# Kernel tuning notes

Measured on AMD Instinct MI355X. Metric: run time of the kernel, lower is better.

Reference implementation:

```python
import jax, jax.numpy as jnp
import numpy as np

LN_EPS = 1e-5
BN_EPS = 1e-5


def setup_inputs() -> dict:
    key = jax.random.key(0)
    ks = jax.random.split(key, 16)
    N, C, T, H, W = 4, 256, 5, 28, 28
    Ci = 128
    CA = 128  # audio feature dim (hard-coded 128 in nn.Linear(128, in_channels))
    s = 0.02
    inp = {
        "x": jax.random.normal(ks[0], (N, C, T, H, W), jnp.float32),
        "audio": jax.random.normal(ks[1], (N, T, CA), jnp.float32),
        "align_W": jax.random.normal(ks[2], (C, CA), jnp.float32) * s,
        "align_b": jax.random.normal(ks[3], (C,), jnp.float32) * s,
        "g_W": jax.random.normal(ks[4], (Ci, C), jnp.float32) * s,
        "g_b": jax.random.normal(ks[5], (Ci,), jnp.float32) * s,
        "theta_W": jax.random.normal(ks[6], (Ci, C), jnp.float32) * s,
        "theta_b": jax.random.normal(ks[7], (Ci,), jnp.float32) * s,
        "phi_W": jax.random.normal(ks[8], (Ci, C), jnp.float32) * s,
        "phi_b": jax.random.normal(ks[9], (Ci,), jnp.float32) * s,
        "Wz_W": jax.random.normal(ks[10], (C, Ci), jnp.float32) * s,
        "Wz_b": jax.random.normal(ks[11], (C,), jnp.float32) * s,
        "bn_gamma": jax.random.normal(ks[12], (C,), jnp.float32) * s + 1.0,
        "bn_beta": jax.random.normal(ks[13], (C,), jnp.float32) * s,
        "bn_mean": jnp.zeros((C,), jnp.float32),
        "bn_var": jnp.ones((C,), jnp.float32),
        "ln_gamma": jnp.ones((C,), jnp.float32),
        "ln_beta": jnp.zeros((C,), jnp.float32),
    }
    return inp


def _tpavi(x, audio, align_W, align_b, g_W, g_b, theta_W, theta_b,
           phi_W, phi_b, Wz_W, Wz_b, bn_gamma, bn_beta, bn_mean, bn_var,
           ln_gamma, ln_beta):
    N, C, T, H, W = x.shape
    L = T * H * W
    # audio alignment: Linear(128 -> C), then broadcast over H, W
    audio_temp = jnp.einsum('ntc,oc->nto', audio, align_W) + align_b     # (N,T,C)
    a = audio_temp.transpose(0, 2, 1)[:, :, :, None, None]               # (N,C,T,1,1)
    a = jnp.broadcast_to(a, (N, C, T, H, W)).reshape(N, C, L)            # (N,C,L)

    xf = x.reshape(N, C, L)                                              # (N,C,L)
    # 1x1 conv3d == per-token channel mixing
    g_x = jnp.einsum('oc,ncl->nlo', g_W, xf) + g_b                       # (N,L,Ci)
    theta_x = jnp.einsum('oc,ncl->nlo', theta_W, xf) + theta_b           # (N,L,Ci)
    phi_x = jnp.einsum('oc,ncl->nol', phi_W, a) + phi_b[None, :, None]   # (N,Ci,L)

    # dot mode: f = theta phi^T, normalized by token count (no softmax)
    f = jnp.einsum('nlo,nok->nlk', theta_x, phi_x)                       # (N,L,L)
    f_div_C = f / L
    y = jnp.einsum('nlk,nko->nlo', f_div_C, g_x)                         # (N,L,Ci)

    y = y.transpose(0, 2, 1)                                             # (N,Ci,L)
    # W_z: 1x1 conv (Ci -> C) + BatchNorm3d (inference statistics)
    wy = jnp.einsum('oc,ncl->nol', Wz_W, y) + Wz_b[None, :, None]        # (N,C,L)
    inv = bn_gamma / jnp.sqrt(bn_var + BN_EPS)
    wy = (wy - bn_mean[None, :, None]) * inv[None, :, None] + bn_beta[None, :, None]

    z = wy.reshape(N, C, T, H, W) + x                                    # residual
    # LayerNorm over channel dim (channels-last in the original)
    zt = z.transpose(0, 2, 3, 4, 1)                                      # (N,T,H,W,C)
    mu = jnp.mean(zt, axis=-1, keepdims=True)
    var = jnp.mean(jnp.square(zt - mu), axis=-1, keepdims=True)
    zt = (zt - mu) / jnp.sqrt(var + LN_EPS) * ln_gamma + ln_beta
    z = zt.transpose(0, 4, 1, 2, 3)                                      # (N,C,T,H,W)
    return z, audio_temp


def reference(x, audio, align_W, align_b, g_W, g_b, theta_W, theta_b,
              phi_W, phi_b, Wz_W, Wz_b, bn_gamma, bn_beta, bn_mean, bn_var,
              ln_gamma, ln_beta):
    return _tpavi(x, audio, align_W, align_b, g_W, g_b, theta_W, theta_b,
                  phi_W, phi_b, Wz_W, Wz_b, bn_gamma, bn_beta, bn_mean, bn_var,
                  ln_gamma, ln_beta)
```

## Files before the change

### kernel.cpp

```cpp
#include <hip/hip_runtime.h>

#define N_DIM 4
#define C_DIM 256
#define T_DIM 5
#define HW    784
#define L_TOK 3920
#define CI    128
#define CA    128

#define WS_XS   0
#define WS_TR   8192

__global__ __launch_bounds__(256) void kA(const float* __restrict__ x,
                                          const float* __restrict__ align_W,
                                          const float* __restrict__ phi_W,
                                          const float* __restrict__ g_W,
                                          const float* __restrict__ Wz_W,
                                          float* __restrict__ ws) {
    int bid = blockIdx.x;
    int tid = threadIdx.x;
    if (bid < N_DIM * C_DIM * T_DIM) {
        int n   = bid / (C_DIM * T_DIM);
        int rem = bid % (C_DIM * T_DIM);
        int c   = rem / T_DIM;
        int t   = rem % T_DIM;
        const float4* base = (const float4*)(x + ((size_t)(n * C_DIM + c) * T_DIM + t) * HW);
        float p = 0.f;
        if (tid < HW / 4) {
            float4 v = base[tid];
            p = (v.x + v.y) + (v.z + v.w);
        }
        for (int off = 32; off > 0; off >>= 1) p += __shfl_down(p, off, 64);
        __shared__ float wsum[4];
        if ((tid & 63) == 0) wsum[tid >> 6] = p;
        __syncthreads();
        if (tid == 0)
            ws[WS_XS + (n * T_DIM + t) * C_DIM + c] = wsum[0] + wsum[1] + wsum[2] + wsum[3];
    } else {
        int tb = bid - N_DIM * C_DIM * T_DIM;
        #pragma unroll
        for (int k = 0; k < 4; ++k) {
            int D = tb * 1024 + k * 256 + tid;
            int m = D >> 15;
            int r = D & 32767;
            float v;
            if (m == 0)      { int a = r >> 8, c = r & 255; v = align_W[c * CA + a]; }
            else if (m == 1) { int c = r >> 7, o = r & 127; v = phi_W[o * C_DIM + c]; }
            else if (m == 2) { int c = r >> 7, o = r & 127; v = g_W[o * C_DIM + c]; }
            else             { int o = r >> 8, c = r & 255; v = Wz_W[c * CI + o]; }
            ws[WS_TR + D] = v;
        }
    }
}

__global__ __launch_bounds__(1024) void kB(
    const float* __restrict__ x,        const float* __restrict__ ws,
    const float* __restrict__ audio,    const float* __restrict__ align_b,
    const float* __restrict__ g_b,      const float* __restrict__ theta_W,
    const float* __restrict__ theta_b,  const float* __restrict__ phi_b,
    const float* __restrict__ Wz_b,     const float* __restrict__ bn_gamma,
    const float* __restrict__ bn_beta,  const float* __restrict__ bn_mean,
    const float* __restrict__ bn_var,   const float* __restrict__ ln_gamma,
    const float* __restrict__ ln_beta,  float* __restrict__ out,
    float* __restrict__ out_audio) {
    __shared__ float audio_s[T_DIM * CA];
    __shared__ float xs_s[T_DIM * C_DIM];
    __shared__ float at_s[T_DIM * C_DIM];
    __shared__ float phi_s[T_DIM * CI];
    __shared__ float g2_s[T_DIM * CI];
    __shared__ float TPs[T_DIM * C_DIM];
    __shared__ float GWs[T_DIM * C_DIM];
    __shared__ float tb_s[T_DIM];
    __shared__ float B_s[C_DIM], inv_s[C_DIM], lng_s[C_DIM], lnb_s[C_DIM];
    __shared__ float Fp[T_DIM * 1024];
    __shared__ float Sp[2 * 1024];

    int n    = blockIdx.y;
    int tile = blockIdx.x;
    int tid  = threadIdx.x;
    int g    = tid >> 6;
    int li   = tid & 63;
    int l    = tile * 64 + li;
    bool act = (l < L_TOK);

    const float* alignT = ws + WS_TR;
    const float* phiT   = ws + WS_TR + 32768;
    const float* gT     = ws + WS_TR + 65536;
    const float* WzT    = ws + WS_TR + 98304;

    if (tid < T_DIM * CA) audio_s[tid] = audio[n * T_DIM * CA + tid];
    for (int i = tid; i < T_DIM * C_DIM; i += 1024) xs_s[i] = ws[WS_XS + n * T_DIM * C_DIM + i];
    if (tid < C_DIM) {
        int c = tid;
        float inv = bn_gamma[c] * rsqrtf(bn_var[c] + 1e-5f);
        inv_s[c] = inv * (1.0f / (float)L_TOK);
        B_s[c]   = (Wz_b[c] - bn_mean[c]) * inv + bn_beta[c];
        lng_s[c] = ln_gamma[c];
        lnb_s[c] = ln_beta[c];
    }
    __syncthreads();

    for (int i = tid; i < T_DIM * C_DIM; i += 1024) {
        int t = i >> 8, c = i & 255;
        float a0 = 0, a1 = 0, a2 = 0, a3 = 0;
        const float* as = audio_s + t * CA;
        #pragma unroll 8
        for (int a = 0; a < CA; a += 4) {
            a0 = fmaf(alignT[(a + 0) * C_DIM + c], as[a + 0], a0);
            a1 = fmaf(alignT[(a + 1) * C_DIM + c], as[a + 1], a1);
            a2 = fmaf(alignT[(a + 2) * C_DIM + c], as[a + 2], a2);
            a3 = fmaf(alignT[(a + 3) * C_DIM + c], as[a + 3], a3);
        }
        float v = align_b[c] + (a0 + a1) + (a2 + a3);
        at_s[i] = v;
        if (tile == 0) out_audio[n * T_DIM * C_DIM + i] = v;
    }
    __syncthreads();

    if (tid < T_DIM * CI) {
        int t = tid >> 7, o = tid & 127;
        const float* ats = at_s + t * C_DIM;
        const float* xss = xs_s + t * C_DIM;
        float p0 = 0, p1 = 0, q0 = 0, q1 = 0;
        #pragma unroll 8
        for (int c = 0; c < C_DIM; c += 2) {
            p0 = fmaf(phiT[(c + 0) * CI + o], ats[c + 0], p0);
            p1 = fmaf(phiT[(c + 1) * CI + o], ats[c + 1], p1);
            q0 = fmaf(gT[(c + 0) * CI + o],  xss[c + 0], q0);
            q1 = fmaf(gT[(c + 1) * CI + o],  xss[c + 1], q1);
        }
        phi_s[tid] = phi_b[o] + p0 + p1;
        g2_s[tid]  = (float)HW * g_b[o] + q0 + q1;
    }
    __syncthreads();

    for (int i = tid; i < T_DIM * C_DIM; i += 1024) {
        int t = i >> 8, c = i & 255;
        const float* ps = phi_s + t * CI;
        const float* gs = g2_s + t * CI;
        float a0 = 0, a1 = 0, b0 = 0, b1 = 0;
        #pragma unroll 8
        for (int o = 0; o < CI; o += 2) {
            a0 = fmaf(theta_W[(o + 0) * C_DIM + c], ps[o + 0], a0);
            a1 = fmaf(theta_W[(o + 1) * C_DIM + c], ps[o + 1], a1);
            b0 = fmaf(WzT[(o + 0) * C_DIM + c],     gs[o + 0], b0);
            b1 = fmaf(WzT[(o + 1) * C_DIM + c],     gs[o + 1], b1);
        }
        TPs[i] = a0 + a1;
        GWs[i] = (b0 + b1) * inv_s[c];
    }
    if (tid < T_DIM * 64) {
        int t = tid >> 6, lane = tid & 63;
        float p = theta_b[lane] * phi_s[t * CI + lane] +
                  theta_b[lane + 64] * phi_s[t * CI + lane + 64];
        for (int off = 32; off > 0; off >>= 1) p += __shfl_down(p, off, 64);
        if (lane == 0) tb_s[t] = p;
    }
    __syncthreads();

    float xz[16];
    const float* xb = x + ((size_t)(n * C_DIM + g * 16)) * L_TOK + l;
    #pragma unroll
    for (int j = 0; j < 16; ++j) xz[j] = act ? xb[(size_t)j * L_TOK] : 0.f;

    float F0 = 0, F1 = 0, F2 = 0, F3 = 0, F4 = 0;
    #pragma unroll
    for (int j = 0; j < 16; ++j) {
        const float* tp = TPs + g * 16 + j;
        F0 = fmaf(xz[j], tp[0],    F0);
        F1 = fmaf(xz[j], tp[256],  F1);
        F2 = fmaf(xz[j], tp[512],  F2);
        F3 = fmaf(xz[j], tp[768],  F3);
        F4 = fmaf(xz[j], tp[1024], F4);
    }
    Fp[0 * 1024 + tid] = F0; Fp[1 * 1024 + tid] = F1; Fp[2 * 1024 + tid] = F2;
    Fp[3 * 1024 + tid] = F3; Fp[4 * 1024 + tid] = F4;
    __syncthreads();

    float Ft[T_DIM];
    #pragma unroll
    for (int t = 0; t < T_DIM; ++t) {
        float a = tb_s[t];
        #pragma unroll
        for (int w = 0; w < 16; ++w) a += Fp[t * 1024 + w * 64 + li];
        Ft[t] = a;
    }
    float s1 = 0.f, s2 = 0.f;
    #pragma unroll
    for (int j = 0; j < 16; ++j) {
        int c = g * 16 + j;
        float zc = B_s[c] + xz[j];
        zc = fmaf(Ft[0], GWs[c],        zc);
        zc = fmaf(Ft[1], GWs[256 + c],  zc);
        zc = fmaf(Ft[2], GWs[512 + c],  zc);
        zc = fmaf(Ft[3], GWs[768 + c],  zc);
        zc = fmaf(Ft[4], GWs[1024 + c], zc);
        xz[j] = zc;
        s1 += zc;
        s2 = fmaf(zc, zc, s2);
    }
    Sp[tid]        = s1;
    Sp[1024 + tid] = s2;
    __syncthreads();

    float t1 = 0.f, t2 = 0.f;
    #pragma unroll
    for (int w = 0; w < 16; ++w) {
        t1 += Sp[w * 64 + li];
        t2 += Sp[1024 + w * 64 + li];
    }
    float mu   = t1 * (1.0f / C_DIM);
    float var  = t2 * (1.0f / C_DIM) - mu * mu;
    float rstd = rsqrtf(var + 1e-5f);
    if (act) {
        float* ob = out + ((size_t)(n * C_DIM + g * 16)) * L_TOK + l;
        #pragma unroll
        for (int j = 0; j < 16; ++j) {
            int c = g * 16 + j;
            ob[(size_t)j * L_TOK] = fmaf((xz[j] - mu) * rstd, lng_s[c], lnb_s[c]);
        }
    }
}

extern "C" void kernel_launch(void* const* d_in, const int* in_sizes, int n_in,
                              void* d_out, int out_size, void* d_ws, size_t ws_size,
                              hipStream_t stream) {
    const float* x        = (const float*)d_in[0];
    const float* audio    = (const float*)d_in[1];
    const float* align_W  = (const float*)d_in[2];
    const float* align_b  = (const float*)d_in[3];
    const float* g_W      = (const float*)d_in[4];
    const float* g_b      = (const float*)d_in[5];
    const float* theta_W  = (const float*)d_in[6];
    const float* theta_b  = (const float*)d_in[7];
    const float* phi_W    = (const float*)d_in[8];
    const float* phi_b    = (const float*)d_in[9];
    const float* Wz_W     = (const float*)d_in[10];
    const float* Wz_b     = (const float*)d_in[11];
    const float* bn_gamma = (const float*)d_in[12];
    const float* bn_beta  = (const float*)d_in[13];
    const float* bn_mean  = (const float*)d_in[14];
    const float* bn_var   = (const float*)d_in[15];
    const float* ln_gamma = (const float*)d_in[16];
    const float* ln_beta  = (const float*)d_in[17];

    float* out       = (float*)d_out;
    float* out_audio = out + (size_t)N_DIM * C_DIM * L_TOK;
    float* ws        = (float*)d_ws;

    kA<<<N_DIM * C_DIM * T_DIM + 128, 256, 0, stream>>>(x, align_W, phi_W, g_W, Wz_W, ws);
    dim3 gridB((L_TOK + 63) / 64, N_DIM);
    kB<<<gridB, 1024, 0, stream>>>(
        x, ws, audio, align_b, g_b, theta_W, theta_b, phi_b,
        Wz_b, bn_gamma, bn_beta, bn_mean, bn_var, ln_gamma, ln_beta,
        out, out_audio);
}
```

Before: 137.5 us.

## Fuse pre-pass into single cooperative kernel with grid-wide sync

Merges the per-(n,t,c) spatial-sum kernel and weight-transpose kernel into the main kernel, launched cooperatively with 248 blocks. Each block loads its x tile into registers once, reduces per-channel partial sums into workspace split at time-step boundaries, then a grid sync lets every block gather the per-time-step sums. This removes one full extra read of x and a kernel launch. The cost is a grid-wide barrier, a serial 62-tile gather in every block, and a dependency on all blocks being co-resident.

```diff
diff --git a/kernel.cpp b/kernel.cpp
--- a/kernel.cpp
+++ b/kernel.cpp
@@ -1,4 +1,7 @@
 #include <hip/hip_runtime.h>
+#include <hip/hip_cooperative_groups.h>
+
+namespace cg = cooperative_groups;
 
 #define N_DIM 4
 #define C_DIM 256
@@ -7,62 +10,19 @@
 #define L_TOK 3920
 #define CI    128
 #define CA    128
-
-#define WS_XS   0
-#define WS_TR   8192
-
-__global__ __launch_bounds__(256) void kA(const float* __restrict__ x,
-                                          const float* __restrict__ align_W,
-                                          const float* __restrict__ phi_W,
-                                          const float* __restrict__ g_W,
-                                          const float* __restrict__ Wz_W,
-                                          float* __restrict__ ws) {
-    int bid = blockIdx.x;
-    int tid = threadIdx.x;
-    if (bid < N_DIM * C_DIM * T_DIM) {
-        int n   = bid / (C_DIM * T_DIM);
-        int rem = bid % (C_DIM * T_DIM);
-        int c   = rem / T_DIM;
-        int t   = rem % T_DIM;
-        const float4* base = (const float4*)(x + ((size_t)(n * C_DIM + c) * T_DIM + t) * HW);
-        float p = 0.f;
-        if (tid < HW / 4) {
-            float4 v = base[tid];
-            p = (v.x + v.y) + (v.z + v.w);
-        }
-        for (int off = 32; off > 0; off >>= 1) p += __shfl_down(p, off, 64);
-        __shared__ float wsum[4];
-        if ((tid & 63) == 0) wsum[tid >> 6] = p;
-        __syncthreads();
-        if (tid == 0)
-            ws[WS_XS + (n * T_DIM + t) * C_DIM + c] = wsum[0] + wsum[1] + wsum[2] + wsum[3];
-    } else {
-        int tb = bid - N_DIM * C_DIM * T_DIM;
-        #pragma unroll
-        for (int k = 0; k < 4; ++k) {
-            int D = tb * 1024 + k * 256 + tid;
-            int m = D >> 15;
-            int r = D & 32767;
-            float v;
-            if (m == 0)      { int a = r >> 8, c = r & 255; v = align_W[c * CA + a]; }
-            else if (m == 1) { int c = r >> 7, o = r & 127; v = phi_W[o * C_DIM + c]; }
-            else if (m == 2) { int c = r >> 7, o = r & 127; v = g_W[o * C_DIM + c]; }
-            else             { int o = r >> 8, c = r & 255; v = Wz_W[c * CI + o]; }
-            ws[WS_TR + D] = v;
-        }
-    }
-}
-
-__global__ __launch_bounds__(1024) void kB(
-    const float* __restrict__ x,        const float* __restrict__ ws,
-    const float* __restrict__ audio,    const float* __restrict__ align_b,
-    const float* __restrict__ g_b,      const float* __restrict__ theta_W,
-    const float* __restrict__ theta_b,  const float* __restrict__ phi_b,
-    const float* __restrict__ Wz_b,     const float* __restrict__ bn_gamma,
-    const float* __restrict__ bn_beta,  const float* __restrict__ bn_mean,
-    const float* __restrict__ bn_var,   const float* __restrict__ ln_gamma,
-    const float* __restrict__ ln_beta,  float* __restrict__ out,
-    float* __restrict__ out_audio) {
+#define NTILE 62
+
+#define WS_TR   0
+#define WS_XP   131072
+
+struct Args {
+    const float *x, *audio, *align_W, *align_b, *g_W, *g_b, *theta_W, *theta_b,
+                *phi_W, *phi_b, *Wz_W, *Wz_b, *bn_gamma, *bn_beta, *bn_mean,
+                *bn_var, *ln_gamma, *ln_beta;
+    float *ws, *out, *out_audio;
+};
+
+__global__ __launch_bounds__(1024) void kFused(Args A) {
     __shared__ float audio_s[T_DIM * CA];
     __shared__ float xs_s[T_DIM * C_DIM];
     __shared__ float at_s[T_DIM * C_DIM];
@@ -75,30 +35,90 @@
     __shared__ float Fp[T_DIM * 1024];
     __shared__ float Sp[2 * 1024];
 
+    int tile = blockIdx.x;
     int n    = blockIdx.y;
-    int tile = blockIdx.x;
+    int bid  = n * NTILE + tile;
     int tid  = threadIdx.x;
     int g    = tid >> 6;
     int li   = tid & 63;
     int l    = tile * 64 + li;
     bool act = (l < L_TOK);
 
+    float* ws = A.ws;
     const float* alignT = ws + WS_TR;
     const float* phiT   = ws + WS_TR + 32768;
     const float* gT     = ws + WS_TR + 65536;
     const float* WzT    = ws + WS_TR + 98304;
 
-    if (tid < T_DIM * CA) audio_s[tid] = audio[n * T_DIM * CA + tid];
-    for (int i = tid; i < T_DIM * C_DIM; i += 1024) xs_s[i] = ws[WS_XS + n * T_DIM * C_DIM + i];
+    {
+        int gid = bid * 1024 + tid;
+        if (gid < 131072) {
+            int m = gid >> 15;
+            int r = gid & 32767;
+            float v;
+            if (m == 0)      { int a = r >> 8, c = r & 255; v = A.align_W[c * CA + a]; }
+            else if (m == 1) { int c = r >> 7, o = r & 127; v = A.phi_W[o * C_DIM + c]; }
+            else if (m == 2) { int c = r >> 7, o = r & 127; v = A.g_W[o * C_DIM + c]; }
+            else             { int o = r >> 8, c = r & 255; v = A.Wz_W[c * CI + o]; }
+            ws[WS_TR + gid] = v;
+        }
+    }
+
+    if (tid < T_DIM * CA) audio_s[tid] = A.audio[n * T_DIM * CA + tid];
     if (tid < C_DIM) {
         int c = tid;
-        float inv = bn_gamma[c] * rsqrtf(bn_var[c] + 1e-5f);
+        float inv = A.bn_gamma[c] * rsqrtf(A.bn_var[c] + 1e-5f);
         inv_s[c] = inv * (1.0f / (float)L_TOK);
-        B_s[c]   = (Wz_b[c] - bn_mean[c]) * inv + bn_beta[c];
-        lng_s[c] = ln_gamma[c];
-        lnb_s[c] = ln_beta[c];
-    }
-    __syncthreads();
+        B_s[c]   = (A.Wz_b[c] - A.bn_mean[c]) * inv + A.bn_beta[c];
+        lng_s[c] = A.ln_gamma[c];
+        lnb_s[c] = A.ln_beta[c];
+    }
+
+    float xz[16];
+    const float* xb = A.x + ((size_t)(n * C_DIM + g * 16)) * L_TOK + l;
+    #pragma unroll
+    for (int j = 0; j < 16; ++j) xz[j] = act ? xb[(size_t)j * L_TOK] : 0.f;
+
+    {
+        int base = tile * 64;
+        int tlo  = base / HW;
+        int thi  = ((base + 63 < L_TOK) ? (base + 63) : (L_TOK - 1)) / HW;
+        int myl  = act ? l : (L_TOK - 1);
+        int mytt = myl / HW;
+        bool straddle = (thi != tlo);
+        float* xp = ws + WS_XP + bid * 512;
+        #pragma unroll
+        for (int j = 0; j < 16; ++j) {
+            float tot = xz[j];
+            for (int off = 32; off > 0; off >>= 1) tot += __shfl_down(tot, off, 64);
+            if (!straddle) {
+                if (li == 0) xp[g * 16 + j] = tot;
+            } else {
+                float v0 = (mytt == tlo) ? xz[j] : 0.f;
+                for (int off = 32; off > 0; off >>= 1) v0 += __shfl_down(v0, off, 64);
+                if (li == 0) {
+                    xp[g * 16 + j]       = v0;
+                    xp[256 + g * 16 + j] = tot - v0;
+                }
+            }
+        }
+    }
+    __threadfence();
+    cg::this_grid().sync();
+
+    for (int i = tid; i < T_DIM * C_DIM; i += 1024) {
+        int t = i >> 8, c = i & 255;
+        float s = 0.f;
+        for (int tt = 0; tt < NTILE; ++tt) {
+            int b2 = tt * 64;
+            int tl = b2 / HW;
+            int th = ((b2 + 63 < L_TOK) ? (b2 + 63) : (L_TOK - 1)) / HW;
+            const float* q = ws + WS_XP + (n * NTILE + tt) * 512;
+            if (t == tl)      s += q[c];
+            else if (t == th) s += q[256 + c];
+        }
+        xs_s[i] = s;
+    }
 
     for (int i = tid; i < T_DIM * C_DIM; i += 1024) {
         int t = i >> 8, c = i & 255;
@@ -111,9 +131,9 @@
             a2 = fmaf(alignT[(a + 2) * C_DIM + c], as[a + 2], a2);
             a3 = fmaf(alignT[(a + 3) * C_DIM + c], as[a + 3], a3);
         }
-        float v = align_b[c] + (a0 + a1) + (a2 + a3);
+        float v = A.align_b[c] + (a0 + a1) + (a2 + a3);
         at_s[i] = v;
-        if (tile == 0) out_audio[n * T_DIM * C_DIM + i] = v;
+        if (tile == 0) A.out_audio[n * T_DIM * C_DIM + i] = v;
     }
     __syncthreads();
 
@@ -129,8 +149,8 @@
             q0 = fmaf(gT[(c + 0) * CI + o],  xss[c + 0], q0);
             q1 = fmaf(gT[(c + 1) * CI + o],  xss[c + 1], q1);
         }
-        phi_s[tid] = phi_b[o] + p0 + p1;
-        g2_s[tid]  = (float)HW * g_b[o] + q0 + q1;
+        phi_s[tid] = A.phi_b[o] + p0 + p1;
+        g2_s[tid]  = (float)HW * A.g_b[o] + q0 + q1;
     }
     __syncthreads();
 
@@ -141,27 +161,22 @@
         float a0 = 0, a1 = 0, b0 = 0, b1 = 0;
         #pragma unroll 8
         for (int o = 0; o < CI; o += 2) {
-            a0 = fmaf(theta_W[(o + 0) * C_DIM + c], ps[o + 0], a0);
-            a1 = fmaf(theta_W[(o + 1) * C_DIM + c], ps[o + 1], a1);
-            b0 = fmaf(WzT[(o + 0) * C_DIM + c],     gs[o + 0], b0);
-            b1 = fmaf(WzT[(o + 1) * C_DIM + c],     gs[o + 1], b1);
+            a0 = fmaf(A.theta_W[(o + 0) * C_DIM + c], ps[o + 0], a0);
+            a1 = fmaf(A.theta_W[(o + 1) * C_DIM + c], ps[o + 1], a1);
+            b0 = fmaf(WzT[(o + 0) * C_DIM + c],       gs[o + 0], b0);
+            b1 = fmaf(WzT[(o + 1) * C_DIM + c],       gs[o + 1], b1);
         }
         TPs[i] = a0 + a1;
         GWs[i] = (b0 + b1) * inv_s[c];
     }
     if (tid < T_DIM * 64) {
         int t = tid >> 6, lane = tid & 63;
-        float p = theta_b[lane] * phi_s[t * CI + lane] +
-                  theta_b[lane + 64] * phi_s[t * CI + lane + 64];
+        float p = A.theta_b[lane] * phi_s[t * CI + lane] +
+                  A.theta_b[lane + 64] * phi_s[t * CI + lane + 64];
         for (int off = 32; off > 0; off >>= 1) p += __shfl_down(p, off, 64);
         if (lane == 0) tb_s[t] = p;
     }
     __syncthreads();
-
-    float xz[16];
-    const float* xb = x + ((size_t)(n * C_DIM + g * 16)) * L_TOK + l;
-    #pragma unroll
-    for (int j = 0; j < 16; ++j) xz[j] = act ? xb[(size_t)j * L_TOK] : 0.f;
 
     float F0 = 0, F1 = 0, F2 = 0, F3 = 0, F4 = 0;
     #pragma unroll
@@ -213,7 +228,7 @@
     float var  = t2 * (1.0f / C_DIM) - mu * mu;
     float rstd = rsqrtf(var + 1e-5f);
     if (act) {
-        float* ob = out + ((size_t)(n * C_DIM + g * 16)) * L_TOK + l;
+        float* ob = A.out + ((size_t)(n * C_DIM + g * 16)) * L_TOK + l;
         #pragma unroll
         for (int j = 0; j < 16; ++j) {
             int c = g * 16 + j;
@@ -225,33 +240,30 @@
 extern "C" void kernel_launch(void* const* d_in, const int* in_sizes, int n_in,
                               void* d_out, int out_size, void* d_ws, size_t ws_size,
                               hipStream_t stream) {
-    const float* x        = (const float*)d_in[0];
-    const float* audio    = (const float*)d_in[1];
-    const float* align_W  = (const float*)d_in[2];
-    const float* align_b  = (const float*)d_in[3];
-    const float* g_W      = (const float*)d_in[4];
-    const float* g_b      = (const float*)d_in[5];
-    const float* theta_W  = (const float*)d_in[6];
-    const float* theta_b  = (const float*)d_in[7];
-    const float* phi_W    = (const float*)d_in[8];
-    const float* phi_b    = (const float*)d_in[9];
-    const float* Wz_W     = (const float*)d_in[10];
-    const float* Wz_b     = (const float*)d_in[11];
-    const float* bn_gamma = (const float*)d_in[12];
-    const float* bn_beta  = (const float*)d_in[13];
-    const float* bn_mean  = (const float*)d_in[14];
-    const float* bn_var   = (const float*)d_in[15];
-    const float* ln_gamma = (const float*)d_in[16];
-    const float* ln_beta  = (const float*)d_in[17];
-
-    float* out       = (float*)d_out;
-    float* out_audio = out + (size_t)N_DIM * C_DIM * L_TOK;
-    float* ws        = (float*)d_ws;
-
-    kA<<<N_DIM * C_DIM * T_DIM + 128, 256, 0, stream>>>(x, align_W, phi_W, g_W, Wz_W, ws);
-    dim3 gridB((L_TOK + 63) / 64, N_DIM);
-    kB<<<gridB, 1024, 0, stream>>>(
-        x, ws, audio, align_b, g_b, theta_W, theta_b, phi_b,
-        Wz_b, bn_gamma, bn_beta, bn_mean, bn_var, ln_gamma, ln_beta,
-        out, out_audio);
+    Args ha;
+    ha.x        = (const float*)d_in[0];
+    ha.audio    = (const float*)d_in[1];
+    ha.align_W  = (const float*)d_in[2];
+    ha.align_b  = (const float*)d_in[3];
+    ha.g_W      = (const float*)d_in[4];
+    ha.g_b      = (const float*)d_in[5];
+    ha.theta_W  = (const float*)d_in[6];
+    ha.theta_b  = (const float*)d_in[7];
+    ha.phi_W    = (const float*)d_in[8];
+    ha.phi_b    = (const float*)d_in[9];
+    ha.Wz_W     = (const float*)d_in[10];
+    ha.Wz_b     = (const float*)d_in[11];
+    ha.bn_gamma = (const float*)d_in[12];
+    ha.bn_beta  = (const float*)d_in[13];
+    ha.bn_mean  = (const float*)d_in[14];
+    ha.bn_var   = (const float*)d_in[15];
+    ha.ln_gamma = (const float*)d_in[16];
+    ha.ln_beta  = (const float*)d_in[17];
+    ha.ws        = (float*)d_ws;
+    ha.out       = (float*)d_out;
+    ha.out_audio = (float*)d_out + (size_t)N_DIM * C_DIM * L_TOK;
+
+    void* kargs[] = { (void*)&ha };
+    hipLaunchCooperativeKernel((const void*)kFused, dim3(NTILE, N_DIM, 1),
+                               dim3(1024, 1, 1), kargs, 0, stream);
 }
```

Result: slower. 282.0 us (+105.0%).
